# Kernel optimization log

Hardware: AMD Instinct MI355X
Metric: run time of the kernel (lower is better)

The kernel has to match this reference:

```python
import jax, jax.numpy as jnp
import numpy as np
from jax import lax

HEAD_DIM = 8          # attention_head_dim
EPS_ATTN = 1e-15
EPS_RMS = 1e-5
KPAD = 2              # kernel_size 5 -> padding 2


def setup_inputs() -> dict:
    key = jax.random.key(0)
    ks = jax.random.split(key, 9)
    B, C, H, W = 2, 1152, 64, 64
    inner = 1152                     # num_heads(144) * head_dim(8)
    ch3 = 3 * inner                  # 3456
    s = 0.02
    return {
        "hidden_states": jax.random.normal(ks[0], (B, C, H, W), jnp.float32),
        "Wq": jax.random.normal(ks[1], (inner, C), jnp.float32) * s,
        "Wk": jax.random.normal(ks[2], (inner, C), jnp.float32) * s,
        "Wv": jax.random.normal(ks[3], (inner, C), jnp.float32) * s,
        "proj_in_w": jax.random.normal(ks[4], (ch3, 1, 5, 5), jnp.float32) * s,   # depthwise 5x5
        "proj_out_w": jax.random.normal(ks[5], (ch3, HEAD_DIM, 1, 1), jnp.float32) * s,  # grouped 1x1, groups=3*heads
        "Wout": jax.random.normal(ks[6], (C, 2 * inner), jnp.float32) * s,
        "rms_w": jnp.ones((C,), jnp.float32),
        "rms_b": jnp.zeros((C,), jnp.float32),
    }


def reference(hidden_states, Wq, Wk, Wv, proj_in_w, proj_out_w, Wout, rms_w, rms_b):
    x = hidden_states
    B, C, H, W = x.shape
    xh = jnp.transpose(x, (0, 2, 3, 1))                      # BHWC
    q = xh @ Wq.T
    k = xh @ Wk.T
    v = xh @ Wv.T
    qkv = jnp.transpose(jnp.concatenate([q, k, v], axis=-1), (0, 3, 1, 2))  # B,3*inner,H,W
    ch = qkv.shape[1]
    # multiscale branch: depthwise 5x5 then grouped 1x1 (groups = 3*num_heads)
    ms = lax.conv_general_dilated(qkv, proj_in_w, (1, 1), [(KPAD, KPAD), (KPAD, KPAD)],
                                  dimension_numbers=("NCHW", "OIHW", "NCHW"),
                                  feature_group_count=ch)
    ms = lax.conv_general_dilated(ms, proj_out_w, (1, 1), [(0, 0), (0, 0)],
                                  dimension_numbers=("NCHW", "OIHW", "NCHW"),
                                  feature_group_count=ch // HEAD_DIM)
    hs = jnp.concatenate([qkv, ms], axis=1).astype(jnp.float32)   # B, 2*3*inner, H, W
    hs = hs.reshape(B, -1, 3 * HEAD_DIM, H * W)                   # B, G, 3d, N
    q2, k2, v2 = jnp.split(hs, 3, axis=2)                         # each B,G,d,N
    q2 = jax.nn.relu(q2)
    k2 = jax.nn.relu(k2)
    # linear attention: pad value with a ones row (for the normalizer)
    v_pad = jnp.concatenate([v2, jnp.ones_like(v2[:, :, :1])], axis=2)  # B,G,d+1,N
    scores = jnp.einsum("bgdn,bgen->bgde", v_pad, k2)             # B,G,d+1,d (tiny)
    out = jnp.einsum("bgde,bgen->bgdn", scores, q2)               # B,G,d+1,N
    out = out[:, :, :-1] / (out[:, :, -1:] + EPS_ATTN)            # normalize by last row
    out = out.reshape(B, -1, H, W)                                # B, 2*inner, H, W
    out = jnp.transpose(out, (0, 2, 3, 1)) @ Wout.T               # BHW,C_out
    # RMSNorm over channel (last) dim, with affine weight + bias
    ms2 = jnp.mean(out * out, axis=-1, keepdims=True)
    out = out * lax.rsqrt(ms2 + EPS_RMS) * rms_w + rms_b
    return jnp.transpose(out, (0, 3, 1, 2))
```

## Files before the change

kernel.cpp:

```cpp
#include <hip/hip_runtime.h>

typedef _Float16 f16;
typedef f16 f16x8 __attribute__((ext_vector_type(8)));
typedef float f32x16 __attribute__((ext_vector_type(16)));

#define NB 2
#define NC 1152
#define NHW 4096
#define NCH3 3456
#define NC2 2304

#define LO_SCALE 2048.0f
#define LO_INV (1.0f / 2048.0f)


__device__ __align__(16) f16 g_Wcat_h[(size_t)NCH3 * NC];
__device__ __align__(16) f16 g_Wcat_l[(size_t)NC * NC];
__device__ __align__(16) f16 g_WoutB_h[(size_t)NC * NC2];
__device__ __align__(16) f16 g_XT_h[(size_t)NB * NHW * NC];
__device__ __align__(16) f16 g_XT_l[(size_t)NB * NHW * NC];
__device__ __align__(16) float g_qkv[(size_t)NB * NCH3 * NHW];
__device__ __align__(16) float g_ms[(size_t)NB * NCH3 * NHW];
__device__ __align__(16) f16 g_attnT_h[(size_t)NB * NHW * NC2];
__device__ float g_part[NB * NHW];

__device__ __forceinline__ void gload16(const void* g, void* l) {
  __builtin_amdgcn_global_load_lds(
      (const __attribute__((address_space(1))) unsigned int*)g,
      (__attribute__((address_space(3))) unsigned int*)l, 16, 0, 0);
}

__device__ __forceinline__ void split_f16(float v, f16& h, f16& l) {
  h = (f16)v;
  l = (f16)((v - (float)h) * LO_SCALE);
}

__global__ __launch_bounds__(256) void convert_weights(
    const float* __restrict__ wq, const float* __restrict__ wk,
    const float* __restrict__ wv, const float* __restrict__ wout) {
  size_t idx = ((size_t)blockIdx.x * 256 + threadIdx.x) * 4;
  const size_t NWC = (size_t)NCH3 * NC;
  const size_t NWO = (size_t)NC * NC2;
  if (idx < NWC) {
    int p = (int)(idx / NC);
    int kk = (int)(idx % NC);
    int role = p / 1152, w = p % 1152;
    int g = w >> 3, r = w & 7;
    int c = g * 24 + role * 8 + r;
    const float* src = (c < 1152) ? wq + (size_t)c * NC + kk
                      : (c < 2304) ? wk + (size_t)(c - 1152) * NC + kk
                                   : wv + (size_t)(c - 2304) * NC + kk;
    if (p < 1152) {
#pragma unroll
      for (int j = 0; j < 4; ++j)
        split_f16(src[j], g_Wcat_h[idx + j], g_Wcat_l[idx + j]);
    } else {
#pragma unroll
      for (int j = 0; j < 4; ++j) g_Wcat_h[idx + j] = (f16)src[j];
    }
  } else {
    size_t k = idx - NWC;
    if (k < NWO) {
      const float* src = wout + k;
#pragma unroll
      for (int j = 0; j < 4; ++j) g_WoutB_h[k + j] = (f16)src[j];
    }
  }
}

__global__ __launch_bounds__(256) void transpose_x(const float* __restrict__ x) {
  __shared__ float tile[32][33];
  int z = blockIdx.z;
  int p0 = blockIdx.x * 32, c0 = blockIdx.y * 32;
  int tx = threadIdx.x, ty = threadIdx.y;
#pragma unroll
  for (int i = 0; i < 32; i += 8)
    tile[ty + i][tx] = x[((size_t)z * NC + c0 + ty + i) * NHW + p0 + tx];
  __syncthreads();
#pragma unroll
  for (int i = 0; i < 32; i += 8) {
    size_t o = ((size_t)z * NHW + p0 + ty + i) * NC + c0 + tx;
    split_f16(tile[tx][ty + i], g_XT_h[o], g_XT_l[o]);
  }
}


__device__ __forceinline__ void gemm1_split_body(char* smem, int bm, int bn, int bz) {
  const int tid = threadIdx.x;
  const int lane = tid & 63;
  const int wid = tid >> 6;
  const int wr = wid >> 2, wc = wid & 3;
  const size_t boff = (size_t)bz * ((size_t)NHW * NC);
  const f16* Bh = g_XT_h + boff;
  const f16* Bl = g_XT_l + boff;
  float* Cb = g_qkv + (size_t)bz * ((size_t)NCH3 * NHW);
  const int srow = tid >> 2;
  const int skb = (((tid & 3) ^ ((srow >> 1) & 3)) * 8);
  const f16* gAh = g_Wcat_h + (size_t)(bm + srow) * NC + skb;
  const f16* gAl = g_Wcat_l + (size_t)(bm + srow) * NC + skb;
  const f16* gBh0 = Bh + (size_t)(bn + srow) * NC + skb;
  const f16* gBl0 = Bl + (size_t)(bn + srow) * NC + skb;
  const f16* gBh1 = Bh + (size_t)(bn + 128 + srow) * NC + skb;
  const f16* gBl1 = Bl + (size_t)(bn + 128 + srow) * NC + skb;
  const int ldso = tid * 16;

  f32x16 acc[2][2] = {};
  f32x16 acc2[2][2] = {};
  const int r31 = lane & 31;
  const int key = (r31 >> 1) & 3;
  const int kblk = lane >> 5;

#define BUF(b, off) (smem + (b) * 49152 + (off))
#define STAGE_S(buf, tile)                                      \
  do {                                                          \
    size_t ko = (size_t)(tile) * 32;                            \
    gload16(gAh + ko, BUF(buf, 0) + ldso);                      \
    gload16(gAl + ko, BUF(buf, 8192) + ldso);                   \
    gload16(gBh0 + ko, BUF(buf, 16384) + ldso);                 \
    gload16(gBh1 + ko, BUF(buf, 24576) + ldso);                 \
    gload16(gBl0 + ko, BUF(buf, 32768) + ldso);                 \
    gload16(gBl1 + ko, BUF(buf, 40960) + ldso);                 \
  } while (0)

#define COMPUTE_S(buf)                                                         \
  do {                                                                         \
    const f16* sAh = (const f16*)BUF(buf, 0);                                  \
    const f16* sAl = (const f16*)BUF(buf, 8192);                               \
    const f16* sBh = (const f16*)BUF(buf, 16384);                              \
    const f16* sBl = (const f16*)BUF(buf, 32768);                              \
    _Pragma("unroll") for (int kh = 0; kh < 2; ++kh) {                         \
      const int bsw = ((kh * 2 + kblk) ^ key) * 8;                             \
      f16x8 ah[2], al[2], bh[2], bl[2];                                        \
      _Pragma("unroll") for (int mb = 0; mb < 2; ++mb) {                       \
        int ro = (wr * 64 + mb * 32 + r31) * 32 + bsw;                         \
        ah[mb] = *(const f16x8*)(sAh + ro);                                    \
        al[mb] = *(const f16x8*)(sAl + ro);                                    \
      }                                                                        \
      _Pragma("unroll") for (int nb = 0; nb < 2; ++nb) {                       \
        int ro = (wc * 64 + nb * 32 + r31) * 32 + bsw;                         \
        bh[nb] = *(const f16x8*)(sBh + ro);                                    \
        bl[nb] = *(const f16x8*)(sBl + ro);                                    \
      }                                                                        \
      __builtin_amdgcn_s_setprio(1);                                           \
      _Pragma("unroll") for (int mb = 0; mb < 2; ++mb)                         \
        _Pragma("unroll") for (int nb = 0; nb < 2; ++nb) {                     \
          acc[mb][nb]  = __builtin_amdgcn_mfma_f32_32x32x16_f16(ah[mb], bh[nb], acc[mb][nb], 0, 0, 0);  \
          acc2[mb][nb] = __builtin_amdgcn_mfma_f32_32x32x16_f16(ah[mb], bl[nb], acc2[mb][nb], 0, 0, 0); \
          acc2[mb][nb] = __builtin_amdgcn_mfma_f32_32x32x16_f16(al[mb], bh[nb], acc2[mb][nb], 0, 0, 0); \
        }                                                                      \
      __builtin_amdgcn_s_setprio(0);                                           \
    }                                                                          \
  } while (0)

  const int NT = NC / 32;
  STAGE_S(0, 0);
  STAGE_S(1, 1);
  int cb = 0, sb = 2;
#pragma unroll 1
  for (int t = 0; t < NT - 1; ++t) {
    asm volatile("s_waitcnt vmcnt(6)" ::: "memory");
    __builtin_amdgcn_s_barrier();
    __builtin_amdgcn_sched_barrier(0);
    if (t + 2 < NT) STAGE_S(sb, t + 2);
    COMPUTE_S(cb);
    __builtin_amdgcn_sched_barrier(0);
    __builtin_amdgcn_s_barrier();
    cb = (cb == 2) ? 0 : cb + 1;
    sb = (sb == 2) ? 0 : sb + 1;
  }
  asm volatile("s_waitcnt vmcnt(0)" ::: "memory");
  __builtin_amdgcn_s_barrier();
  __builtin_amdgcn_sched_barrier(0);
  COMPUTE_S(cb);
#undef STAGE_S
#undef COMPUTE_S
#undef BUF
#pragma unroll
  for (int mb = 0; mb < 2; ++mb)
#pragma unroll
    for (int nb = 0; nb < 2; ++nb) {
      int col = bn + wc * 64 + nb * 32 + r31;
#pragma unroll
      for (int reg = 0; reg < 16; ++reg) {
        int row = bm + wr * 64 + mb * 32 + (reg & 3) + 8 * (reg >> 2) + 4 * (lane >> 5);
        Cb[(size_t)row * NHW + col] = acc[mb][nb][reg] + acc2[mb][nb][reg] * LO_INV;
      }
    }
}

__device__ __forceinline__ void gemm1_plain_body(char* smem, int bm, int bn, int bz) {
  const int tid = threadIdx.x;
  const int lane = tid & 63;
  const int wid = tid >> 6;
  const int wr = wid >> 2, wc = wid & 3;
  const size_t boff = (size_t)bz * ((size_t)NHW * NC);
  const f16* Bh = g_XT_h + boff;
  float* Cb = g_qkv + (size_t)bz * ((size_t)NCH3 * NHW);
  const int srow = tid >> 2;
  const int skb = (((tid & 3) ^ ((srow >> 1) & 3)) * 8);
  const f16* gA = g_Wcat_h + (size_t)(bm + srow) * NC + skb;
  const f16* gB0 = Bh + (size_t)(bn + srow) * NC + skb;
  const f16* gB1 = Bh + (size_t)(bn + 128 + srow) * NC + skb;
  const int ldso = tid * 16;

  f32x16 acc[2][2] = {};
  const int r31 = lane & 31;
  const int key = (r31 >> 1) & 3;
  const int kblk = lane >> 5;

#define BUF(b, off) (smem + (b) * 24576 + (off))
#define STAGE_Q(buf, tile)                                      \
  do {                                                          \
    size_t ko = (size_t)(tile) * 32;                            \
    gload16(gA + ko, BUF(buf, 0) + ldso);                       \
    gload16(gB0 + ko, BUF(buf, 8192) + ldso);                   \
    gload16(gB1 + ko, BUF(buf, 16384) + ldso);                  \
  } while (0)

#define COMPUTE_Q(buf)                                                         \
  do {                                                                         \
    const f16* sA = (const f16*)BUF(buf, 0);                                   \
    const f16* sB = (const f16*)BUF(buf, 8192);                                \
    _Pragma("unroll") for (int kh = 0; kh < 2; ++kh) {                         \
      const int bsw = ((kh * 2 + kblk) ^ key) * 8;                             \
      f16x8 af[2], bf[2];                                                      \
      _Pragma("unroll") for (int mb = 0; mb < 2; ++mb)                         \
        af[mb] = *(const f16x8*)(sA + (wr * 64 + mb * 32 + r31) * 32 + bsw);   \
      _Pragma("unroll") for (int nb = 0; nb < 2; ++nb)                         \
        bf[nb] = *(const f16x8*)(sB + (wc * 64 + nb * 32 + r31) * 32 + bsw);   \
      __builtin_amdgcn_s_setprio(1);                                           \
      _Pragma("unroll") for (int mb = 0; mb < 2; ++mb)                         \
        _Pragma("unroll") for (int nb = 0; nb < 2; ++nb)                       \
          acc[mb][nb] = __builtin_amdgcn_mfma_f32_32x32x16_f16(af[mb], bf[nb], acc[mb][nb], 0, 0, 0); \
      __builtin_amdgcn_s_setprio(0);                                           \
    }                                                                          \
  } while (0)

  const int NT = NC / 32;
  STAGE_Q(0, 0);
  STAGE_Q(1, 1);
  int cb = 0, sb = 2;
#pragma unroll 1
  for (int t = 0; t < NT - 1; ++t) {
    asm volatile("s_waitcnt vmcnt(3)" ::: "memory");
    __builtin_amdgcn_s_barrier();
    __builtin_amdgcn_sched_barrier(0);
    if (t + 2 < NT) STAGE_Q(sb, t + 2);
    COMPUTE_Q(cb);
    __builtin_amdgcn_sched_barrier(0);
    __builtin_amdgcn_s_barrier();
    cb = (cb == 2) ? 0 : cb + 1;
    sb = (sb == 2) ? 0 : sb + 1;
  }
  asm volatile("s_waitcnt vmcnt(0)" ::: "memory");
  __builtin_amdgcn_s_barrier();
  __builtin_amdgcn_sched_barrier(0);
  COMPUTE_Q(cb);
#undef STAGE_Q
#undef COMPUTE_Q
#undef BUF
#pragma unroll
  for (int mb = 0; mb < 2; ++mb)
#pragma unroll
    for (int nb = 0; nb < 2; ++nb) {
      int col = bn + wc * 64 + nb * 32 + r31;
#pragma unroll
      for (int reg = 0; reg < 16; ++reg) {
        int row = bm + wr * 64 + mb * 32 + (reg & 3) + 8 * (reg >> 2) + 4 * (lane >> 5);
        Cb[(size_t)row * NHW + col] = acc[mb][nb][reg];
      }
    }
}

__global__ __launch_bounds__(512, 1) void gemm1_kernel() {
  __shared__ __align__(16) char smem[147456];
  int bid = blockIdx.x;
  int swz = (bid & 7) * 108 + (bid >> 3);
  int bx = swz % 27, rem = swz / 27;
  int by = rem & 15, bz = rem >> 4;
  if (bx < 9)
    gemm1_split_body(smem, bx * 128, by * 256, bz);
  else
    gemm1_plain_body(smem, bx * 128, by * 256, bz);
}

template <int M, int N, int K>
__device__ __forceinline__ void gemm_body_plain(
    const f16* __restrict__ A, const f16* __restrict__ Bt,
    float* __restrict__ C, int bm, int bn, int bz) {
  __shared__ __align__(16) f16 sA[3][128 * 32];
  __shared__ __align__(16) f16 sB[3][128 * 32];
  const int tid = threadIdx.x;
  const int lane = tid & 63;
  const int wid = tid >> 6;
  const int wr = wid >> 1, wc = wid & 1;
  const f16* Bb = Bt + (size_t)bz * ((size_t)N * K);
  float* Cb = C + (size_t)bz * ((size_t)M * N);
  const int srow = tid >> 2;
  const int skb = (((tid & 3) ^ ((srow >> 1) & 3)) * 8);
  const f16* gA0 = A + (size_t)(bm + srow) * K + skb;
  const f16* gA1 = A + (size_t)(bm + 64 + srow) * K + skb;
  const f16* gB0 = Bb + (size_t)(bn + srow) * K + skb;
  const f16* gB1 = Bb + (size_t)(bn + 64 + srow) * K + skb;
  const int ldso = tid * 16;

  f32x16 acc[2][2] = {};
  const int r31 = lane & 31;
  const int key = (r31 >> 1) & 3;
  const int kblk = lane >> 5;

#define STAGE_P(buf, tile)                              \
  do {                                                  \
    size_t ko = (size_t)(tile) * 32;                    \
    gload16(gA0 + ko, (char*)sA[buf] + ldso);           \
    gload16(gA1 + ko, (char*)sA[buf] + 4096 + ldso);    \
    gload16(gB0 + ko, (char*)sB[buf] + ldso);           \
    gload16(gB1 + ko, (char*)sB[buf] + 4096 + ldso);    \
  } while (0)

#define COMPUTE_P(buf)                                                         \
  do {                                                                         \
    _Pragma("unroll") for (int kh = 0; kh < 2; ++kh) {                         \
      const int bsw = ((kh * 2 + kblk) ^ key) * 8;                             \
      f16x8 af[2], bf[2];                                                      \
      _Pragma("unroll") for (int mb = 0; mb < 2; ++mb)                         \
        af[mb] = *(const f16x8*)(sA[buf] + (wr * 64 + mb * 32 + r31) * 32 + bsw); \
      _Pragma("unroll") for (int nb = 0; nb < 2; ++nb)                         \
        bf[nb] = *(const f16x8*)(sB[buf] + (wc * 64 + nb * 32 + r31) * 32 + bsw); \
      __builtin_amdgcn_s_setprio(1);                                           \
      _Pragma("unroll") for (int mb = 0; mb < 2; ++mb)                         \
        _Pragma("unroll") for (int nb = 0; nb < 2; ++nb)                       \
          acc[mb][nb] = __builtin_amdgcn_mfma_f32_32x32x16_f16(af[mb], bf[nb], acc[mb][nb], 0, 0, 0); \
      __builtin_amdgcn_s_setprio(0);                                           \
    }                                                                          \
  } while (0)

  const int NT = K / 32;
  STAGE_P(0, 0);
  STAGE_P(1, 1);
  int cb = 0, sb = 2;
#pragma unroll 1
  for (int t = 0; t < NT - 1; ++t) {
    asm volatile("s_waitcnt vmcnt(4)" ::: "memory");
    __builtin_amdgcn_s_barrier();
    __builtin_amdgcn_sched_barrier(0);
    if (t + 2 < NT) STAGE_P(sb, t + 2);
    COMPUTE_P(cb);
    __builtin_amdgcn_sched_barrier(0);
    __builtin_amdgcn_s_barrier();
    cb = (cb == 2) ? 0 : cb + 1;
    sb = (sb == 2) ? 0 : sb + 1;
  }
  asm volatile("s_waitcnt vmcnt(0)" ::: "memory");
  __builtin_amdgcn_s_barrier();
  __builtin_amdgcn_sched_barrier(0);
  COMPUTE_P(cb);
#undef STAGE_P
#undef COMPUTE_P
#pragma unroll
  for (int nb = 0; nb < 2; ++nb) {
    int col = bn + wc * 64 + nb * 32 + r31;
    float csum = 0.f;
#pragma unroll
    for (int mb = 0; mb < 2; ++mb)
#pragma unroll
      for (int reg = 0; reg < 16; ++reg) {
        int row = bm + wr * 64 + mb * 32 + (reg & 3) + 8 * (reg >> 2) + 4 * (lane >> 5);
        float v = acc[mb][nb][reg];
        Cb[(size_t)row * N + col] = v;
        csum += v * v;
      }
    atomicAdd(&g_part[bz * NHW + col], csum);
  }
}

__global__ __launch_bounds__(256, 2) void gemm2_kernel(float* __restrict__ out) {
  int bid = blockIdx.x;
  int swz = (bid & 7) * (576 / 8) + (bid >> 3);
  int bx = swz % 9, rem = swz / 9;
  int by = rem & 31, bz = rem >> 5;
  gemm_body_plain<NC, NHW, NC2>(g_WoutB_h, g_attnT_h, out,
                                bx * 128, by * 128, bz);
}

__global__ __launch_bounds__(256) void conv_kernel(const float* __restrict__ wdw,
                                                   const float* __restrict__ wpw) {
  const int z = blockIdx.z, gg = blockIdx.y;
  const int pbase = (gg % 3) * 1152 + (gg / 3) * 8;
  const int px = blockIdx.x * 2048 + threadIdx.x * 8;
  const int h = px >> 6, w0 = px & 63;
  const float* base = g_qkv + ((size_t)z * NCH3 + pbase) * NHW;

  float dw[8][8];
#pragma unroll
  for (int ci = 0; ci < 8; ++ci) {
    const float* wd = wdw + (gg * 8 + ci) * 25;
    const float* srcc = base + (size_t)ci * NHW;
    float acc[8] = {};
#pragma unroll
    for (int dy = -2; dy <= 2; ++dy) {
      int hh = h + dy;
      if (hh < 0 || hh > 63) continue;
      const float* row = srcc + hh * 64;
      float4 Lv = (w0 >= 4) ? *(const float4*)(row + w0 - 4)
                            : make_float4(0.f, 0.f, 0.f, 0.f);
      float4 M0 = *(const float4*)(row + w0);
      float4 M1 = *(const float4*)(row + w0 + 4);
      float4 Rv = (w0 <= 52) ? *(const float4*)(row + w0 + 8)
                             : make_float4(0.f, 0.f, 0.f, 0.f);
      float c[16] = {Lv.x, Lv.y, Lv.z, Lv.w, M0.x, M0.y, M0.z, M0.w,
                     M1.x, M1.y, M1.z, M1.w, Rv.x, Rv.y, Rv.z, Rv.w};
      const float* wrow = wd + (dy + 2) * 5;
#pragma unroll
      for (int dx = 0; dx < 5; ++dx) {
        float wv = wrow[dx];
#pragma unroll
        for (int j = 0; j < 8; ++j) acc[j] += c[2 + dx + j] * wv;
      }
    }
#pragma unroll
    for (int j = 0; j < 8; ++j) dw[ci][j] = acc[j];
  }
#pragma unroll
  for (int o = 0; o < 8; ++o) {
    const float* wp = wpw + (size_t)(gg * 8 + o) * 8;
    float out[8] = {};
#pragma unroll
    for (int i = 0; i < 8; ++i) {
      float wv = wp[i];
#pragma unroll
      for (int j = 0; j < 8; ++j) out[j] += wv * dw[i][j];
    }
    float* dst = g_ms + ((size_t)z * NCH3 + pbase + o) * NHW + px;
    *(float4*)dst = make_float4(out[0], out[1], out[2], out[3]);
    *(float4*)(dst + 4) = make_float4(out[4], out[5], out[6], out[7]);
  }
}

__global__ __launch_bounds__(256) void attn_kernel() {
  int g = blockIdx.x;
  int z = blockIdx.y;
  int tid = threadIdx.x;
  const float* buf = (g < 144) ? g_qkv : g_ms;
  int gq = (g < 144) ? g : g - 144;
  const float* qp = buf + ((size_t)z * NCH3 + gq * 8) * NHW;
  const float* kp = buf + ((size_t)z * NCH3 + 1152 + gq * 8) * NHW;
  const float* vp = buf + ((size_t)z * NCH3 + 2304 + gq * 8) * NHW;

  float s[9][8];
#pragma unroll
  for (int d = 0; d < 9; ++d)
#pragma unroll
    for (int e = 0; e < 8; ++e) s[d][e] = 0.f;

  for (int p = tid; p < NHW; p += 256) {
    float kv[8], vv[8];
#pragma unroll
    for (int e = 0; e < 8; ++e) kv[e] = fmaxf(kp[(size_t)e * NHW + p], 0.f);
#pragma unroll
    for (int d = 0; d < 8; ++d) vv[d] = vp[(size_t)d * NHW + p];
#pragma unroll
    for (int e = 0; e < 8; ++e) {
#pragma unroll
      for (int d = 0; d < 8; ++d) s[d][e] += vv[d] * kv[e];
      s[8][e] += kv[e];
    }
  }
#pragma unroll
  for (int d = 0; d < 9; ++d)
#pragma unroll
    for (int e = 0; e < 8; ++e) {
      float v = s[d][e];
#pragma unroll
      for (int off = 32; off > 0; off >>= 1) v += __shfl_xor(v, off, 64);
      s[d][e] = v;
    }
  __shared__ float sred[4][72];
  __shared__ float sc[72];
  int w = tid >> 6, lane = tid & 63;
  if (lane == 0) {
#pragma unroll
    for (int d = 0; d < 9; ++d)
#pragma unroll
      for (int e = 0; e < 8; ++e) sred[w][d * 8 + e] = s[d][e];
  }
  __syncthreads();
  if (tid < 72) sc[tid] = sred[0][tid] + sred[1][tid] + sred[2][tid] + sred[3][tid];
  __syncthreads();
  float scl[9][8];
#pragma unroll
  for (int d = 0; d < 9; ++d)
#pragma unroll
    for (int e = 0; e < 8; ++e) scl[d][e] = sc[d * 8 + e];

  for (int p = tid; p < NHW; p += 256) {
    float qv[8];
#pragma unroll
    for (int e = 0; e < 8; ++e) qv[e] = fmaxf(qp[(size_t)e * NHW + p], 0.f);
    float o[9];
#pragma unroll
    for (int d = 0; d < 9; ++d) {
      float a = 0.f;
#pragma unroll
      for (int e = 0; e < 8; ++e) a += scl[d][e] * qv[e];
      o[d] = a;
    }
    float r = 1.f / (o[8] + 1e-15f);
    f16x8 oh;
#pragma unroll
    for (int d = 0; d < 8; ++d) oh[d] = (f16)(o[d] * r);
    *(f16x8*)(g_attnT_h + ((size_t)z * NHW + p) * NC2 + g * 8) = oh;
  }
}

__global__ __launch_bounds__(256) void rms_zero() {
  g_part[blockIdx.x * 256 + threadIdx.x] = 0.f;
}
__global__ __launch_bounds__(256) void rms_norm(float* __restrict__ y,
                                                const float* __restrict__ w,
                                                const float* __restrict__ b) {
  size_t i = ((size_t)blockIdx.x * 256 + threadIdx.x) * 4;
  float4 v = *(const float4*)(y + i);
  int p = (int)(i & (NHW - 1));
  int c = (int)((i >> 12) % NC);
  int z = (int)(i / ((size_t)NC * NHW));
  const float inv = 1.0f / NC;
  float wc = w[c], bc = b[c];
  const float* pp = &g_part[z * NHW + p];
  v.x = v.x * rsqrtf(pp[0] * inv + 1e-5f) * wc + bc;
  v.y = v.y * rsqrtf(pp[1] * inv + 1e-5f) * wc + bc;
  v.z = v.z * rsqrtf(pp[2] * inv + 1e-5f) * wc + bc;
  v.w = v.w * rsqrtf(pp[3] * inv + 1e-5f) * wc + bc;
  *(float4*)(y + i) = v;
}

extern "C" void kernel_launch(void* const* d_in, const int* in_sizes, int n_in,
                              void* d_out, int out_size, void* d_ws, size_t ws_size,
                              hipStream_t stream) {
  const float* x = (const float*)d_in[0];
  const float* wq = (const float*)d_in[1];
  const float* wk = (const float*)d_in[2];
  const float* wv = (const float*)d_in[3];
  const float* wdw = (const float*)d_in[4];
  const float* wpw = (const float*)d_in[5];
  const float* wout = (const float*)d_in[6];
  const float* rw = (const float*)d_in[7];
  const float* rb = (const float*)d_in[8];
  float* y = (float*)d_out;

  convert_weights<<<6480, 256, 0, stream>>>(wq, wk, wv, wout);
  transpose_x<<<dim3(128, 36, 2), dim3(32, 8), 0, stream>>>(x);
  gemm1_kernel<<<864, 512, 0, stream>>>();
  conv_kernel<<<dim3(2, 432, 2), 256, 0, stream>>>(wdw, wpw);
  attn_kernel<<<dim3(288, 2), 256, 0, stream>>>();
  rms_zero<<<32, 256, 0, stream>>>();
  gemm2_kernel<<<576, 256, 0, stream>>>(y);
  rms_norm<<<9216, 256, 0, stream>>>(y, rw, rb);
}
```

Before: 458.1 us.

## Store qkv and multiscale intermediates in fp16 and vectorize conv/attn loads

The qkv and multiscale intermediate buffers change from fp32 to fp16. The GEMM epilogue, the depthwise conv and the attention kernels are updated to write and read half-width data, using 8-wide vector loads. This cuts global memory traffic for the large intermediates, which are about 56 MB each in fp32. The trade-off is lower precision in the intermediates, plus less coalesced per-pixel output writes in the attention kernel since each thread now handles 8 consecutive pixels.

```diff
diff --git a/kernel.cpp b/kernel.cpp
--- a/kernel.cpp
+++ b/kernel.cpp
@@ -19,8 +19,8 @@
 __device__ __align__(16) f16 g_WoutB_h[(size_t)NC * NC2];
 __device__ __align__(16) f16 g_XT_h[(size_t)NB * NHW * NC];
 __device__ __align__(16) f16 g_XT_l[(size_t)NB * NHW * NC];
-__device__ __align__(16) float g_qkv[(size_t)NB * NCH3 * NHW];
-__device__ __align__(16) float g_ms[(size_t)NB * NCH3 * NHW];
+__device__ __align__(16) f16 g_qkv[(size_t)NB * NCH3 * NHW];
+__device__ __align__(16) f16 g_ms[(size_t)NB * NCH3 * NHW];
 __device__ __align__(16) f16 g_attnT_h[(size_t)NB * NHW * NC2];
 __device__ float g_part[NB * NHW];
 
@@ -93,7 +93,7 @@
   const size_t boff = (size_t)bz * ((size_t)NHW * NC);
   const f16* Bh = g_XT_h + boff;
   const f16* Bl = g_XT_l + boff;
-  float* Cb = g_qkv + (size_t)bz * ((size_t)NCH3 * NHW);
+  f16* Cb = g_qkv + (size_t)bz * ((size_t)NCH3 * NHW);
   const int srow = tid >> 2;
   const int skb = (((tid & 3) ^ ((srow >> 1) & 3)) * 8);
   const f16* gAh = g_Wcat_h + (size_t)(bm + srow) * NC + skb;
@@ -183,7 +183,7 @@
 #pragma unroll
       for (int reg = 0; reg < 16; ++reg) {
         int row = bm + wr * 64 + mb * 32 + (reg & 3) + 8 * (reg >> 2) + 4 * (lane >> 5);
-        Cb[(size_t)row * NHW + col] = acc[mb][nb][reg] + acc2[mb][nb][reg] * LO_INV;
+        Cb[(size_t)row * NHW + col] = (f16)(acc[mb][nb][reg] + acc2[mb][nb][reg] * LO_INV);
       }
     }
 }
@@ -195,7 +195,7 @@
   const int wr = wid >> 2, wc = wid & 3;
   const size_t boff = (size_t)bz * ((size_t)NHW * NC);
   const f16* Bh = g_XT_h + boff;
-  float* Cb = g_qkv + (size_t)bz * ((size_t)NCH3 * NHW);
+  f16* Cb = g_qkv + (size_t)bz * ((size_t)NCH3 * NHW);
   const int srow = tid >> 2;
   const int skb = (((tid & 3) ^ ((srow >> 1) & 3)) * 8);
   const f16* gA = g_Wcat_h + (size_t)(bm + srow) * NC + skb;
@@ -267,7 +267,7 @@
 #pragma unroll
       for (int reg = 0; reg < 16; ++reg) {
         int row = bm + wr * 64 + mb * 32 + (reg & 3) + 8 * (reg >> 2) + 4 * (lane >> 5);
-        Cb[(size_t)row * NHW + col] = acc[mb][nb][reg];
+        Cb[(size_t)row * NHW + col] = (f16)acc[mb][nb][reg];
       }
     }
 }
@@ -389,33 +389,36 @@
   const int pbase = (gg % 3) * 1152 + (gg / 3) * 8;
   const int px = blockIdx.x * 2048 + threadIdx.x * 8;
   const int h = px >> 6, w0 = px & 63;
-  const float* base = g_qkv + ((size_t)z * NCH3 + pbase) * NHW;
+  const f16* base = g_qkv + ((size_t)z * NCH3 + pbase) * NHW;
 
   float dw[8][8];
 #pragma unroll
   for (int ci = 0; ci < 8; ++ci) {
     const float* wd = wdw + (gg * 8 + ci) * 25;
-    const float* srcc = base + (size_t)ci * NHW;
+    const f16* srcc = base + (size_t)ci * NHW;
     float acc[8] = {};
 #pragma unroll
     for (int dy = -2; dy <= 2; ++dy) {
       int hh = h + dy;
       if (hh < 0 || hh > 63) continue;
-      const float* row = srcc + hh * 64;
-      float4 Lv = (w0 >= 4) ? *(const float4*)(row + w0 - 4)
-                            : make_float4(0.f, 0.f, 0.f, 0.f);
-      float4 M0 = *(const float4*)(row + w0);
-      float4 M1 = *(const float4*)(row + w0 + 4);
-      float4 Rv = (w0 <= 52) ? *(const float4*)(row + w0 + 8)
-                             : make_float4(0.f, 0.f, 0.f, 0.f);
-      float c[16] = {Lv.x, Lv.y, Lv.z, Lv.w, M0.x, M0.y, M0.z, M0.w,
-                     M1.x, M1.y, M1.z, M1.w, Rv.x, Rv.y, Rv.z, Rv.w};
+      const f16* row = srcc + hh * 64;
+      f16x8 Lv = {}, Rv = {};
+      if (w0 >= 8) Lv = *(const f16x8*)(row + w0 - 8);
+      f16x8 Mv = *(const f16x8*)(row + w0);
+      if (w0 <= 48) Rv = *(const f16x8*)(row + w0 + 8);
+      float c[24];
+#pragma unroll
+      for (int i = 0; i < 8; ++i) {
+        c[i] = (float)Lv[i];
+        c[8 + i] = (float)Mv[i];
+        c[16 + i] = (float)Rv[i];
+      }
       const float* wrow = wd + (dy + 2) * 5;
 #pragma unroll
       for (int dx = 0; dx < 5; ++dx) {
         float wv = wrow[dx];
 #pragma unroll
-        for (int j = 0; j < 8; ++j) acc[j] += c[2 + dx + j] * wv;
+        for (int j = 0; j < 8; ++j) acc[j] += c[6 + j + dx] * wv;
       }
     }
 #pragma unroll
@@ -431,9 +434,10 @@
 #pragma unroll
       for (int j = 0; j < 8; ++j) out[j] += wv * dw[i][j];
     }
-    float* dst = g_ms + ((size_t)z * NCH3 + pbase + o) * NHW + px;
-    *(float4*)dst = make_float4(out[0], out[1], out[2], out[3]);
-    *(float4*)(dst + 4) = make_float4(out[4], out[5], out[6], out[7]);
+    f16x8 ov;
+#pragma unroll
+    for (int j = 0; j < 8; ++j) ov[j] = (f16)out[j];
+    *(f16x8*)(g_ms + ((size_t)z * NCH3 + pbase + o) * NHW + px) = ov;
   }
 }
 
@@ -441,11 +445,11 @@
   int g = blockIdx.x;
   int z = blockIdx.y;
   int tid = threadIdx.x;
-  const float* buf = (g < 144) ? g_qkv : g_ms;
+  const f16* buf = (g < 144) ? g_qkv : g_ms;
   int gq = (g < 144) ? g : g - 144;
-  const float* qp = buf + ((size_t)z * NCH3 + gq * 8) * NHW;
-  const float* kp = buf + ((size_t)z * NCH3 + 1152 + gq * 8) * NHW;
-  const float* vp = buf + ((size_t)z * NCH3 + 2304 + gq * 8) * NHW;
+  const f16* qp = buf + ((size_t)z * NCH3 + gq * 8) * NHW;
+  const f16* kp = buf + ((size_t)z * NCH3 + 1152 + gq * 8) * NHW;
+  const f16* vp = buf + ((size_t)z * NCH3 + 2304 + gq * 8) * NHW;
 
   float s[9][8];
 #pragma unroll
@@ -453,17 +457,25 @@
 #pragma unroll
     for (int e = 0; e < 8; ++e) s[d][e] = 0.f;
 
-  for (int p = tid; p < NHW; p += 256) {
-    float kv[8], vv[8];
-#pragma unroll
-    for (int e = 0; e < 8; ++e) kv[e] = fmaxf(kp[(size_t)e * NHW + p], 0.f);
-#pragma unroll
-    for (int d = 0; d < 8; ++d) vv[d] = vp[(size_t)d * NHW + p];
-#pragma unroll
-    for (int e = 0; e < 8; ++e) {
-#pragma unroll
-      for (int d = 0; d < 8; ++d) s[d][e] += vv[d] * kv[e];
-      s[8][e] += kv[e];
+  for (int p0 = tid * 8; p0 < NHW; p0 += 2048) {
+    f16x8 kx[8], vx[8];
+#pragma unroll
+    for (int e = 0; e < 8; ++e) kx[e] = *(const f16x8*)(kp + (size_t)e * NHW + p0);
+#pragma unroll
+    for (int d = 0; d < 8; ++d) vx[d] = *(const f16x8*)(vp + (size_t)d * NHW + p0);
+#pragma unroll
+    for (int j = 0; j < 8; ++j) {
+      float kv[8], vv[8];
+#pragma unroll
+      for (int e = 0; e < 8; ++e) kv[e] = fmaxf((float)kx[e][j], 0.f);
+#pragma unroll
+      for (int d = 0; d < 8; ++d) vv[d] = (float)vx[d][j];
+#pragma unroll
+      for (int e = 0; e < 8; ++e) {
+#pragma unroll
+        for (int d = 0; d < 8; ++d) s[d][e] += vv[d] * kv[e];
+        s[8][e] += kv[e];
+      }
     }
   }
 #pragma unroll
@@ -493,23 +505,29 @@
 #pragma unroll
     for (int e = 0; e < 8; ++e) scl[d][e] = sc[d * 8 + e];
 
-  for (int p = tid; p < NHW; p += 256) {
-    float qv[8];
-#pragma unroll
-    for (int e = 0; e < 8; ++e) qv[e] = fmaxf(qp[(size_t)e * NHW + p], 0.f);
-    float o[9];
-#pragma unroll
-    for (int d = 0; d < 9; ++d) {
-      float a = 0.f;
-#pragma unroll
-      for (int e = 0; e < 8; ++e) a += scl[d][e] * qv[e];
-      o[d] = a;
-    }
-    float r = 1.f / (o[8] + 1e-15f);
-    f16x8 oh;
-#pragma unroll
-    for (int d = 0; d < 8; ++d) oh[d] = (f16)(o[d] * r);
-    *(f16x8*)(g_attnT_h + ((size_t)z * NHW + p) * NC2 + g * 8) = oh;
+  for (int p0 = tid * 8; p0 < NHW; p0 += 2048) {
+    f16x8 qx[8];
+#pragma unroll
+    for (int e = 0; e < 8; ++e) qx[e] = *(const f16x8*)(qp + (size_t)e * NHW + p0);
+#pragma unroll
+    for (int j = 0; j < 8; ++j) {
+      float qv[8];
+#pragma unroll
+      for (int e = 0; e < 8; ++e) qv[e] = fmaxf((float)qx[e][j], 0.f);
+      float o[9];
+#pragma unroll
+      for (int d = 0; d < 9; ++d) {
+        float a = 0.f;
+#pragma unroll
+        for (int e = 0; e < 8; ++e) a += scl[d][e] * qv[e];
+        o[d] = a;
+      }
+      float r = 1.f / (o[8] + 1e-15f);
+      f16x8 oh;
+#pragma unroll
+      for (int d = 0; d < 8; ++d) oh[d] = (f16)(o[d] * r);
+      *(f16x8*)(g_attnT_h + ((size_t)z * NHW + p0 + j) * NC2 + g * 8) = oh;
+    }
   }
 }
 
```

Measured after the change: 399.0 us. 1.15x faster.
